# Optimization experiments

Hardware: AMD Instinct MI355X
Metric: run time of the kernel (lower is better)

Reference implementation:

```python
import jax, jax.numpy as jnp
import numpy as np

NUMBASIS = 10
OFFSET = jnp.linspace(-3.0, 3.0, NUMBASIS)
COEFF = -0.5 / (OFFSET[1] - OFFSET[0]) ** 2
CR_CR_MEAN, CR_CR_STD = 4.0, 0.16
CR_I_MEAN, CR_I_STD = 2.8, 0.035
ANGLE_MEAN, ANGLE_STD = -0.025, 0.06

E, N, G = 1_000_000, 250_000, 512

def _rbf(x):
    # x: [E, 1] -> [E, NUMBASIS]; PyG GaussianSmearing
    d = x - OFFSET
    return jnp.exp(COEFF * d * d)

def _layernorm(x, g, b, eps=1e-5):
    mu = jnp.mean(x, axis=-1, keepdims=True)
    xc = x - mu
    var = jnp.mean(xc * xc, axis=-1, keepdims=True)
    return xc * jax.lax.rsqrt(var + eps) * g + b

def setup_inputs() -> dict:
    key = jax.random.key(0)
    ks = jax.random.split(key, 16)
    def w(k, shape):
        return jax.random.normal(k, shape, jnp.float32) / np.sqrt(shape[0])
    return {
        "edge_src": jax.random.randint(ks[0], (E,), 0, N),
        "edge_dst": jax.random.randint(ks[1], (E,), 0, N),
        "batch_idx": jnp.sort(jax.random.randint(ks[2], (N,), 0, G)),
        "cell": jax.random.normal(ks[3], (G, 3, 3), jnp.float32),
        "edge_shift": jax.random.normal(ks[4], (E, 3), jnp.float32),
        "pos": jax.random.normal(ks[5], (N, 3), jnp.float32),
        "angles": jax.random.normal(ks[6], (E,), jnp.float32),
        "cr_i_bonds": jax.random.normal(ks[7], (E, 4), jnp.float32),
        "ln_g": jnp.ones((60,), jnp.float32),
        "ln_b": jnp.zeros((60,), jnp.float32),
        "wn1": w(ks[8], (60, 32)), "bn1": jnp.zeros((32,), jnp.float32),
        "wn2": w(ks[9], (32, 1)), "bn2": jnp.zeros((1,), jnp.float32),
        "we1": w(ks[10], (60, 64)), "be1": jnp.zeros((64,), jnp.float32),
        "we2": w(ks[11], (64, 1)), "be2": jnp.zeros((1,), jnp.float32),
        "wr1": w(ks[12], (60, 32)), "br1": jnp.zeros((32,), jnp.float32),
        "wr2": w(ks[13], (32, 2)), "br2": jnp.zeros((2,), jnp.float32),
    }

def reference(edge_src, edge_dst, batch_idx, cell, edge_shift, pos, angles,
              cr_i_bonds, ln_g, ln_b, wn1, bn1, wn2, bn2, we1, be1, we2, be2,
              wr1, br1, wr2, br2):
    gidx = batch_idx[edge_src]                      # [E]
    bcell = cell[gidx]                              # [E,3,3]
    tvec = jnp.einsum('ei,eij->ej', edge_shift, bcell)
    radvec = pos[edge_dst] - pos[edge_src] + tvec   # [E,3]
    dist = jnp.linalg.norm(radvec, axis=1, keepdims=True)  # [E,1]
    ang = angles.reshape(-1, 1)
    dist_z = (dist - CR_CR_MEAN) / CR_CR_STD
    ang_z = (ang - ANGLE_MEAN) / ANGLE_STD
    legs_z = (cr_i_bonds - CR_I_MEAN) / CR_I_STD    # [E,4]
    emb = jnp.concatenate([
        _rbf(dist_z), _rbf(ang_z),
        _rbf(legs_z[:, 0:1]), _rbf(legs_z[:, 1:2]),
        _rbf(legs_z[:, 2:3]), _rbf(legs_z[:, 3:4]),
    ], axis=-1)                                     # [E,60]
    h = _layernorm(emb, ln_g, ln_b)
    # dropout layers are identity in eval mode
    routing = jax.nn.softmax(jax.nn.silu(h @ wr1 + br1) @ wr2 + br2, axis=-1)
    pred_normal = jax.nn.silu(h @ wn1 + bn1) @ wn2 + bn2   # [E,1]
    pred_extreme = jax.nn.silu(h @ we1 + be1) @ we2 + be2  # [E,1]
    out = routing[:, 0:1] * pred_normal + routing[:, 1:2] * pred_extreme
    return out.reshape(-1)
```

## Files before the change

### kernel.cpp

```cpp
#include <hip/hip_runtime.h>
#include <math.h>

#define E_THREADS 128
#define EPB 128

typedef __attribute__((ext_vector_type(8))) short short8;
typedef __attribute__((ext_vector_type(4))) float floatx4;


#define A_L2E 1.6230319f

__device__ inline unsigned short f2bf(float f) {
    union { float f; unsigned u; } v; v.f = f;
    unsigned r = v.u + 0x7FFFu + ((v.u >> 16) & 1u);
    return (unsigned short)(r >> 16);
}

__device__ inline unsigned cvt_pk_bf16(float lo, float hi) {
    unsigned r;
    asm("v_cvt_pk_bf16_f32 %0, %1, %2" : "=v"(r) : "v"(lo), "v"(hi));
    return r;
}

__device__ inline float fexp2(float x) { return __builtin_amdgcn_exp2f(x); }
__device__ inline float frcp(float x)  { return __builtin_amdgcn_rcpf(x); }
#define LOG2E 1.44269504f

__global__ __launch_bounds__(256)
void prep_weights(
    const float* __restrict__ ln_g, const float* __restrict__ ln_b,
    const float* __restrict__ wn1, const float* __restrict__ bn1,
    const float* __restrict__ wn2, const float* __restrict__ bn2,
    const float* __restrict__ we1, const float* __restrict__ be1,
    const float* __restrict__ we2, const float* __restrict__ be2,
    const float* __restrict__ wr1, const float* __restrict__ br1,
    const float* __restrict__ wr2, const float* __restrict__ br2,
    char* __restrict__ ws)
{
    uint4* WF  = (uint4*)ws;
    float* W2A = (float*)(ws + 16384);
    float* W2B = (float*)(ws + 16896);
    float* SC  = (float*)(ws + 17024);
    const int tid = threadIdx.x;

    for (int idx = tid; idx < 1024; idx += 256) {
        int u = idx >> 7, s = (idx >> 6) & 1, lane = idx & 63;
        int lcol = lane & 15, khi = lane >> 4;
        int n = 16 * u + lcol;
        int kbase = s * 32 + khi * 8;
        float w8[8];
        for (int j = 0; j < 8; ++j) {
            int k = kbase + j;
            float w = 0.0f;
            if (k < 60) {
                float wv = (n < 32) ? wn1[k * 32 + n]
                         : (n < 96) ? we1[k * 64 + (n - 32)]
                                    : wr1[k * 32 + (n - 96)];
                w = ln_g[k] * wv;
            } else if (k == 60) {
                float b = (n < 32) ? bn1[n] : (n < 96) ? be1[n - 32] : br1[n - 96];
                for (int kk = 0; kk < 60; ++kk) {
                    float wv = (n < 32) ? wn1[kk * 32 + n]
                             : (n < 96) ? we1[kk * 64 + (n - 32)]
                                        : wr1[kk * 32 + (n - 96)];
                    b += ln_b[kk] * wv;
                }
                w = b;
            }
            w8[j] = w;
        }
        unsigned q0 = (unsigned)f2bf(w8[0]) | ((unsigned)f2bf(w8[1]) << 16);
        unsigned q1 = (unsigned)f2bf(w8[2]) | ((unsigned)f2bf(w8[3]) << 16);
        unsigned q2 = (unsigned)f2bf(w8[4]) | ((unsigned)f2bf(w8[5]) << 16);
        unsigned q3 = (unsigned)f2bf(w8[6]) | ((unsigned)f2bf(w8[7]) << 16);
        WF[idx] = make_uint4(q0, q1, q2, q3);
    }
    if (tid < 128) {
        int n = tid;
        W2A[n] = (n < 32) ? wn2[n] : (n < 96) ? we2[n - 32] : wr2[(n - 96) * 2];
    }
    if (tid >= 128 && tid < 160) W2B[tid - 128] = wr2[(tid - 128) * 2 + 1];
    if (tid == 0) { SC[0] = bn2[0]; SC[1] = be2[0]; SC[2] = br2[0]; SC[3] = br2[1]; }
}

__attribute__((amdgpu_waves_per_eu(4, 5)))
__global__ __launch_bounds__(E_THREADS, 4)
void exchange_block_kernel(
    const int*   __restrict__ edge_src,
    const int*   __restrict__ edge_dst,
    const int*   __restrict__ batch_idx,
    const float* __restrict__ cell,
    const float* __restrict__ edge_shift,
    const float* __restrict__ pos,
    const float* __restrict__ angles,
    const float* __restrict__ cr_bonds,
    const char*  __restrict__ ws,
    float* __restrict__ out, int E)
{
    __shared__ __align__(16) unsigned short HLDS[EPB * 64];
    __shared__ __align__(16) float LW2A[128];
    __shared__ __align__(16) float LW2B[32];

    const int tid = threadIdx.x;
    const int e = blockIdx.x * EPB + tid;

    LW2A[tid] = ((const float*)(ws + 16384))[tid];
    if (tid < 32) LW2B[tid] = ((const float*)(ws + 16896))[tid];

    float h[64];
    if (e < E) {
        int s = edge_src[e];
        int d = edge_dst[e];
        int g = batch_idx[s];
        float sh0 = edge_shift[e * 3 + 0];
        float sh1 = edge_shift[e * 3 + 1];
        float sh2 = edge_shift[e * 3 + 2];
        const float* c = cell + g * 9;
        float t0 = sh0 * c[0] + sh1 * c[3] + sh2 * c[6];
        float t1 = sh0 * c[1] + sh1 * c[4] + sh2 * c[7];
        float t2 = sh0 * c[2] + sh1 * c[5] + sh2 * c[8];
        float r0 = pos[d * 3 + 0] - pos[s * 3 + 0] + t0;
        float r1 = pos[d * 3 + 1] - pos[s * 3 + 1] + t1;
        float r2 = pos[d * 3 + 2] - pos[s * 3 + 2] + t2;
        float dist = sqrtf(r0 * r0 + r1 * r1 + r2 * r2);

        float z[6];
        z[0] = (dist - 4.0f) * (1.0f / 0.16f);
        z[1] = (angles[e] + 0.025f) * (1.0f / 0.06f);
        z[2] = (cr_bonds[e * 4 + 0] - 2.8f) * (1.0f / 0.035f);
        z[3] = (cr_bonds[e * 4 + 1] - 2.8f) * (1.0f / 0.035f);
        z[4] = (cr_bonds[e * 4 + 2] - 2.8f) * (1.0f / 0.035f);
        z[5] = (cr_bonds[e * 4 + 3] - 2.8f) * (1.0f / 0.035f);

        #pragma unroll
        for (int gi = 0; gi < 6; ++gi) {
            float zv = fminf(13.0f, fmaxf(-13.0f, z[gi]));
            float tt = zv + 3.0f;
            float hv = fexp2(-A_L2E * tt * tt);
            float rv = fexp2(fmaf(zv, 2.1640426f, 5.7707802f));
            h[gi * 10] = hv;
            #pragma unroll
            for (int k = 1; k < 10; ++k) {
                hv *= rv;
                rv *= 0.36787944f;
                h[gi * 10 + k] = hv;
            }
        }
        float mu = 0.0f;
        #pragma unroll
        for (int k = 0; k < 60; ++k) mu += h[k];
        mu *= (1.0f / 60.0f);
        float var = 0.0f;
        #pragma unroll
        for (int k = 0; k < 60; ++k) { float xc = h[k] - mu; var += xc * xc; }
        var *= (1.0f / 60.0f);
        float rs = rsqrtf(var + 1e-5f);
        float nmurs = -mu * rs;
        #pragma unroll
        for (int k = 0; k < 60; ++k) h[k] = fmaf(h[k], rs, nmurs);
    } else {
        #pragma unroll
        for (int k = 0; k < 60; ++k) h[k] = 0.0f;
    }
    h[60] = 1.0f;
    h[61] = 0.0f; h[62] = 0.0f; h[63] = 0.0f;

    {
        const int swz = (tid & 7) << 4;
        #pragma unroll
        for (int c = 0; c < 8; ++c) {
            unsigned q0 = cvt_pk_bf16(h[8 * c + 0], h[8 * c + 1]);
            unsigned q1 = cvt_pk_bf16(h[8 * c + 2], h[8 * c + 3]);
            unsigned q2 = cvt_pk_bf16(h[8 * c + 4], h[8 * c + 5]);
            unsigned q3 = cvt_pk_bf16(h[8 * c + 6], h[8 * c + 7]);
            *(uint4*)((char*)HLDS + tid * 128 + ((c * 16) ^ swz)) = make_uint4(q0, q1, q2, q3);
        }
    }
    __syncthreads();

    const uint4* WF = (const uint4*)ws;
    const float* SC = (const float*)(ws + 17024);

    const int lane = tid & 63;
    const int wv   = tid >> 6;
    const int lcol = lane & 15;
    const int khi  = lane >> 4;
    const int kof  = khi * 16;

    uint4 wf[16];
    #pragma unroll
    for (int i = 0; i < 16; ++i) wf[i] = WF[i * 64 + lane];
    #pragma unroll
    for (int i = 0; i < 16; ++i)
        asm volatile("" : "+v"(wf[i].x), "+v"(wf[i].y), "+v"(wf[i].z), "+v"(wf[i].w));

    const float bn2v = SC[0], be2v = SC[1], br2v0 = SC[2], br2v1 = SC[3];

    #pragma unroll
    for (int t = 0; t < 4; ++t) {
        const int hrow = wv * 64 + t * 16 + lcol;
        const char* hbase = (const char*)HLDS + hrow * 128;
        const int hswz = (hrow & 7) << 4;
        short8 b0 = *(const short8*)(hbase + ((0  + kof) ^ hswz));
        short8 b1 = *(const short8*)(hbase + ((64 + kof) ^ hswz));

        float sN = 0.0f, sE = 0.0f, sR0 = 0.0f, sR1 = 0.0f;
        #pragma unroll
        for (int u = 0; u < 8; ++u) {
            short8 a0 = *(const short8*)&wf[u * 2 + 0];
            short8 a1 = *(const short8*)&wf[u * 2 + 1];
            floatx4 acc = (floatx4){0.0f, 0.0f, 0.0f, 0.0f};
            acc = __builtin_amdgcn_mfma_f32_16x16x32_bf16(a0, b0, acc, 0, 0, 0);
            acc = __builtin_amdgcn_mfma_f32_16x16x32_bf16(a1, b1, acc, 0, 0, 0);

            float4 w2 = *(const float4*)&LW2A[16 * u + khi * 4];
            const float* w2p = (const float*)&w2;
            float4 wb4;
            const float* wbp = (const float*)&wb4;
            if (u >= 6) wb4 = *(const float4*)&LW2B[(u - 6) * 16 + khi * 4];
            #pragma unroll
            for (int j = 0; j < 4; ++j) {
                float a  = acc[j];
                float sl = a * frcp(1.0f + fexp2(a * -LOG2E));
                float w  = w2p[j];
                if (u < 2)      sN += sl * w;
                else if (u < 6) sE += sl * w;
                else {
                    sR0 += sl * w;
                    sR1 += sl * wbp[j];
                }
            }
        }
        sN  += __shfl_xor(sN,  16); sN  += __shfl_xor(sN,  32);
        sE  += __shfl_xor(sE,  16); sE  += __shfl_xor(sE,  32);
        sR0 += __shfl_xor(sR0, 16); sR0 += __shfl_xor(sR0, 32);
        sR1 += __shfl_xor(sR1, 16); sR1 += __shfl_xor(sR1, 32);

        sN += bn2v; sE += be2v; sR0 += br2v0; sR1 += br2v1;
        float rt = frcp(1.0f + fexp2((sR1 - sR0) * LOG2E));
        float val = sE + rt * (sN - sE);

        if (lane < 16) {
            int eb = blockIdx.x * EPB + wv * 64 + t * 16 + lcol;
            if (eb < E) out[eb] = val;
        }
    }
}

extern "C" void kernel_launch(void* const* d_in, const int* in_sizes, int n_in,
                              void* d_out, int out_size, void* d_ws, size_t ws_size,
                              hipStream_t stream)
{
    const int*   edge_src  = (const int*)  d_in[0];
    const int*   edge_dst  = (const int*)  d_in[1];
    const int*   batch_idx = (const int*)  d_in[2];
    const float* cell      = (const float*)d_in[3];
    const float* edge_shift= (const float*)d_in[4];
    const float* pos       = (const float*)d_in[5];
    const float* angles    = (const float*)d_in[6];
    const float* cr_bonds  = (const float*)d_in[7];
    const float* ln_g      = (const float*)d_in[8];
    const float* ln_b      = (const float*)d_in[9];
    const float* wn1 = (const float*)d_in[10]; const float* bn1 = (const float*)d_in[11];
    const float* wn2 = (const float*)d_in[12]; const float* bn2 = (const float*)d_in[13];
    const float* we1 = (const float*)d_in[14]; const float* be1 = (const float*)d_in[15];
    const float* we2 = (const float*)d_in[16]; const float* be2 = (const float*)d_in[17];
    const float* wr1 = (const float*)d_in[18]; const float* br1 = (const float*)d_in[19];
    const float* wr2 = (const float*)d_in[20]; const float* br2 = (const float*)d_in[21];

    int E = in_sizes[0];
    float* out = (float*)d_out;

    hipLaunchKernelGGL(prep_weights, dim3(1), dim3(256), 0, stream,
                       ln_g, ln_b, wn1, bn1, wn2, bn2, we1, be1, we2, be2,
                       wr1, br1, wr2, br2, (char*)d_ws);

    int grid = (E + EPB - 1) / EPB;
    hipLaunchKernelGGL(exchange_block_kernel, dim3(grid), dim3(E_THREADS), 0, stream,
                       edge_src, edge_dst, batch_idx, cell, edge_shift, pos,
                       angles, cr_bonds, (const char*)d_ws, out, E);
}
```

Measured before the change: 83.70 us.

## Interchange MLP loops to stream weights, split reductions, and coalesce output store

The layernorm mean and variance sums now use eight partial accumulators, which shortens the serial add dependency chains. The MFMA loop is inverted: all four edge tiles' B fragments are loaded from LDS up front, and each weight fragment is streamed from global inside the outer loop instead of pinning all 16 in registers. This cuts weight register pressure but adds per-tile accumulators, and it gives the MFMA and SiLU work more independent instructions to overlap. The final store is also restructured so every lane writes one output in a single coalesced store, replacing four partial-lane stores.

New measurement: 146.5 us. +75.0%, slower.

```diff
diff --git a/kernel.cpp b/kernel.cpp
--- a/kernel.cpp
+++ b/kernel.cpp
@@ -146,13 +146,27 @@
                 h[gi * 10 + k] = hv;
             }
         }
-        float mu = 0.0f;
-        #pragma unroll
-        for (int k = 0; k < 60; ++k) mu += h[k];
+        float mp[8] = {0.f,0.f,0.f,0.f,0.f,0.f,0.f,0.f};
+        #pragma unroll
+        for (int k = 0; k < 56; k += 8)
+            #pragma unroll
+            for (int j = 0; j < 8; ++j) mp[j] += h[k + j];
+        mp[0] += h[56]; mp[1] += h[57]; mp[2] += h[58]; mp[3] += h[59];
+        float mu = ((mp[0] + mp[1]) + (mp[2] + mp[3]))
+                 + ((mp[4] + mp[5]) + (mp[6] + mp[7]));
         mu *= (1.0f / 60.0f);
-        float var = 0.0f;
-        #pragma unroll
-        for (int k = 0; k < 60; ++k) { float xc = h[k] - mu; var += xc * xc; }
+        float vp[8] = {0.f,0.f,0.f,0.f,0.f,0.f,0.f,0.f};
+        #pragma unroll
+        for (int k = 0; k < 56; k += 8)
+            #pragma unroll
+            for (int j = 0; j < 8; ++j) { float xc = h[k + j] - mu; vp[j] += xc * xc; }
+        { float xc;
+          xc = h[56] - mu; vp[0] += xc * xc;
+          xc = h[57] - mu; vp[1] += xc * xc;
+          xc = h[58] - mu; vp[2] += xc * xc;
+          xc = h[59] - mu; vp[3] += xc * xc; }
+        float var = ((vp[0] + vp[1]) + (vp[2] + vp[3]))
+                  + ((vp[4] + vp[5]) + (vp[6] + vp[7]));
         var *= (1.0f / 60.0f);
         float rs = rsqrtf(var + 1e-5f);
         float nmurs = -mu * rs;
@@ -178,8 +192,8 @@
     }
     __syncthreads();
 
-    const uint4* WF = (const uint4*)ws;
-    const float* SC = (const float*)(ws + 17024);
+    const short8* WF = (const short8*)ws;
+    const float*  SC = (const float*)(ws + 17024);
 
     const int lane = tid & 63;
     const int wv   = tid >> 6;
@@ -187,63 +201,106 @@
     const int khi  = lane >> 4;
     const int kof  = khi * 16;
 
-    uint4 wf[16];
-    #pragma unroll
-    for (int i = 0; i < 16; ++i) wf[i] = WF[i * 64 + lane];
-    #pragma unroll
-    for (int i = 0; i < 16; ++i)
-        asm volatile("" : "+v"(wf[i].x), "+v"(wf[i].y), "+v"(wf[i].z), "+v"(wf[i].w));
-
-    const float bn2v = SC[0], be2v = SC[1], br2v0 = SC[2], br2v1 = SC[3];
-
+    short8 bf[4][2];
     #pragma unroll
     for (int t = 0; t < 4; ++t) {
         const int hrow = wv * 64 + t * 16 + lcol;
         const char* hbase = (const char*)HLDS + hrow * 128;
         const int hswz = (hrow & 7) << 4;
-        short8 b0 = *(const short8*)(hbase + ((0  + kof) ^ hswz));
-        short8 b1 = *(const short8*)(hbase + ((64 + kof) ^ hswz));
-
-        float sN = 0.0f, sE = 0.0f, sR0 = 0.0f, sR1 = 0.0f;
-        #pragma unroll
-        for (int u = 0; u < 8; ++u) {
-            short8 a0 = *(const short8*)&wf[u * 2 + 0];
-            short8 a1 = *(const short8*)&wf[u * 2 + 1];
-            floatx4 acc = (floatx4){0.0f, 0.0f, 0.0f, 0.0f};
-            acc = __builtin_amdgcn_mfma_f32_16x16x32_bf16(a0, b0, acc, 0, 0, 0);
-            acc = __builtin_amdgcn_mfma_f32_16x16x32_bf16(a1, b1, acc, 0, 0, 0);
-
-            float4 w2 = *(const float4*)&LW2A[16 * u + khi * 4];
-            const float* w2p = (const float*)&w2;
-            float4 wb4;
-            const float* wbp = (const float*)&wb4;
-            if (u >= 6) wb4 = *(const float4*)&LW2B[(u - 6) * 16 + khi * 4];
+        bf[t][0] = *(const short8*)(hbase + ((0  + kof) ^ hswz));
+        bf[t][1] = *(const short8*)(hbase + ((64 + kof) ^ hswz));
+    }
+
+    float sN[4]  = {0.f, 0.f, 0.f, 0.f};
+    float sE0[4] = {0.f, 0.f, 0.f, 0.f};
+    float sE1[4] = {0.f, 0.f, 0.f, 0.f};
+    float sR0[4] = {0.f, 0.f, 0.f, 0.f};
+    float sR1[4] = {0.f, 0.f, 0.f, 0.f};
+
+    #pragma unroll
+    for (int u = 0; u < 2; ++u) {
+        short8 a0 = WF[(u * 2 + 0) * 64 + lane];
+        short8 a1 = WF[(u * 2 + 1) * 64 + lane];
+        float4 w2 = *(const float4*)&LW2A[16 * u + khi * 4];
+        const float* w2p = (const float*)&w2;
+        #pragma unroll
+        for (int t = 0; t < 4; ++t) {
+            floatx4 acc = (floatx4){0.f, 0.f, 0.f, 0.f};
+            acc = __builtin_amdgcn_mfma_f32_16x16x32_bf16(a0, bf[t][0], acc, 0, 0, 0);
+            acc = __builtin_amdgcn_mfma_f32_16x16x32_bf16(a1, bf[t][1], acc, 0, 0, 0);
             #pragma unroll
             for (int j = 0; j < 4; ++j) {
                 float a  = acc[j];
                 float sl = a * frcp(1.0f + fexp2(a * -LOG2E));
-                float w  = w2p[j];
-                if (u < 2)      sN += sl * w;
-                else if (u < 6) sE += sl * w;
-                else {
-                    sR0 += sl * w;
-                    sR1 += sl * wbp[j];
-                }
-            }
-        }
-        sN  += __shfl_xor(sN,  16); sN  += __shfl_xor(sN,  32);
-        sE  += __shfl_xor(sE,  16); sE  += __shfl_xor(sE,  32);
-        sR0 += __shfl_xor(sR0, 16); sR0 += __shfl_xor(sR0, 32);
-        sR1 += __shfl_xor(sR1, 16); sR1 += __shfl_xor(sR1, 32);
-
-        sN += bn2v; sE += be2v; sR0 += br2v0; sR1 += br2v1;
-        float rt = frcp(1.0f + fexp2((sR1 - sR0) * LOG2E));
-        float val = sE + rt * (sN - sE);
-
-        if (lane < 16) {
-            int eb = blockIdx.x * EPB + wv * 64 + t * 16 + lcol;
-            if (eb < E) out[eb] = val;
-        }
+                sN[t] += sl * w2p[j];
+            }
+        }
+    }
+    #pragma unroll
+    for (int u = 2; u < 6; ++u) {
+        short8 a0 = WF[(u * 2 + 0) * 64 + lane];
+        short8 a1 = WF[(u * 2 + 1) * 64 + lane];
+        float4 w2 = *(const float4*)&LW2A[16 * u + khi * 4];
+        const float* w2p = (const float*)&w2;
+        #pragma unroll
+        for (int t = 0; t < 4; ++t) {
+            floatx4 acc = (floatx4){0.f, 0.f, 0.f, 0.f};
+            acc = __builtin_amdgcn_mfma_f32_16x16x32_bf16(a0, bf[t][0], acc, 0, 0, 0);
+            acc = __builtin_amdgcn_mfma_f32_16x16x32_bf16(a1, bf[t][1], acc, 0, 0, 0);
+            #pragma unroll
+            for (int j = 0; j < 4; ++j) {
+                float a  = acc[j];
+                float sl = a * frcp(1.0f + fexp2(a * -LOG2E));
+                if (u & 1) sE1[t] += sl * w2p[j];
+                else       sE0[t] += sl * w2p[j];
+            }
+        }
+    }
+    #pragma unroll
+    for (int u = 6; u < 8; ++u) {
+        short8 a0 = WF[(u * 2 + 0) * 64 + lane];
+        short8 a1 = WF[(u * 2 + 1) * 64 + lane];
+        float4 w2 = *(const float4*)&LW2A[16 * u + khi * 4];
+        float4 wb = *(const float4*)&LW2B[(u - 6) * 16 + khi * 4];
+        const float* w2p = (const float*)&w2;
+        const float* wbp = (const float*)&wb;
+        #pragma unroll
+        for (int t = 0; t < 4; ++t) {
+            floatx4 acc = (floatx4){0.f, 0.f, 0.f, 0.f};
+            acc = __builtin_amdgcn_mfma_f32_16x16x32_bf16(a0, bf[t][0], acc, 0, 0, 0);
+            acc = __builtin_amdgcn_mfma_f32_16x16x32_bf16(a1, bf[t][1], acc, 0, 0, 0);
+            #pragma unroll
+            for (int j = 0; j < 4; ++j) {
+                float a  = acc[j];
+                float sl = a * frcp(1.0f + fexp2(a * -LOG2E));
+                sR0[t] += sl * w2p[j];
+                sR1[t] += sl * wbp[j];
+            }
+        }
+    }
+
+    const float bn2v = SC[0], be2v = SC[1], br2v0 = SC[2], br2v1 = SC[3];
+
+    float val[4];
+    #pragma unroll
+    for (int t = 0; t < 4; ++t) {
+        float vN  = sN[t],  vE  = sE0[t] + sE1[t];
+        float vR0 = sR0[t], vR1 = sR1[t];
+        vN  += __shfl_xor(vN,  16); vN  += __shfl_xor(vN,  32);
+        vE  += __shfl_xor(vE,  16); vE  += __shfl_xor(vE,  32);
+        vR0 += __shfl_xor(vR0, 16); vR0 += __shfl_xor(vR0, 32);
+        vR1 += __shfl_xor(vR1, 16); vR1 += __shfl_xor(vR1, 32);
+
+        vN += bn2v; vE += be2v; vR0 += br2v0; vR1 += br2v1;
+        float rt = frcp(1.0f + fexp2((vR1 - vR0) * LOG2E));
+        val[t] = vE + rt * (vN - vE);
+    }
+
+    {
+        float v = (khi == 0) ? val[0] : (khi == 1) ? val[1]
+                : (khi == 2) ? val[2] : val[3];
+        int eb = blockIdx.x * EPB + wv * 64 + khi * 16 + lcol;
+        if (eb < E) out[eb] = v;
     }
 }
 
```
